# Optimization experiments

Measured on AMD Instinct MI355X. Metric: run time of the kernel, lower is better.

Reference implementation:

```python
import jax, jax.numpy as jnp
import numpy as np

B, S, E = 2048, 23, 768
RED, H, NUM_LABELS = 256, 8, 25
DH = RED // H
DELTA = 0.1
EPS_LN = 1e-5


def setup_inputs() -> dict:
    key = jax.random.key(0)
    ks = jax.random.split(key, 20)
    g = lambda k, shape, fan: jax.random.normal(k, shape, dtype=jnp.float32) * (1.0 / np.sqrt(fan))
    inp = {
        'cls_embeddings': jax.random.normal(ks[0], (B, S, E), dtype=jnp.float32),
        'existing_mask': jax.random.randint(ks[1], (B, S), 0, 2, dtype=jnp.int32),
        'missing_emb': g(ks[2], (S, E), E),
        'W1': g(ks[3], (E // 2, E), E), 'b1': jnp.zeros((E // 2,), jnp.float32),
        'W2': g(ks[4], (RED, E // 2), E // 2), 'b2': jnp.zeros((RED,), jnp.float32),
        'ln_g': jnp.ones((RED,), jnp.float32), 'ln_b': jnp.zeros((RED,), jnp.float32),
        'Wq': g(ks[5], (RED, RED), RED), 'bq': jnp.zeros((RED,), jnp.float32),
        'Wk': g(ks[6], (RED, RED), RED), 'bk': jnp.zeros((RED,), jnp.float32),
        'Wv': g(ks[7], (RED, RED), RED), 'bv': jnp.zeros((RED,), jnp.float32),
        'Wo': g(ks[8], (RED, RED), RED), 'bo': jnp.zeros((RED,), jnp.float32),
        'Wp': g(ks[9], (NUM_LABELS, RED), RED), 'bp': jnp.zeros((NUM_LABELS,), jnp.float32),
    }
    return inp


def _layer_norm(x, g, b):
    mu = jnp.mean(x, axis=-1, keepdims=True)
    var = jnp.mean(jnp.square(x - mu), axis=-1, keepdims=True)
    return (x - mu) * jax.lax.rsqrt(var + EPS_LN) * g + b


def _forward(cls_embeddings, existing_mask, missing_emb, W1, b1, W2, b2, ln_g, ln_b,
             Wq, bq, Wk, bk, Wv, bv, Wo, bo, Wp, bp):
    exist = existing_mask > 0                              # [B,S] bool
    # Gather: existing sections use BERT CLS, missing slots use learned embeddings
    sec = jnp.where(exist[..., None], cls_embeddings, missing_emb[None])  # [B,S,E]
    # SectionDimReducer (exact-erf GELU as in nn.GELU default)
    h = jax.nn.gelu(sec @ W1.T + b1, approximate=False)
    h = jax.nn.gelu(h @ W2.T + b2, approximate=False)
    red = _layer_norm(h, ln_g, ln_b)                       # [B,S,RED]
    # Tiny MHA: every slot queries the existing sections of its own EHR
    q = (red @ Wq.T + bq).reshape(B, S, H, DH)
    k = (red @ Wk.T + bk).reshape(B, S, H, DH)
    v = (red @ Wv.T + bv).reshape(B, S, H, DH)
    scores = jnp.einsum('bqhd,bkhd->bhqk', q, k) / np.sqrt(DH)
    scores = jnp.where(exist[:, None, None, :], scores, -1e9)
    attn = jax.nn.softmax(scores, axis=-1)                 # [B,H,S,S]
    ctx = jnp.einsum('bhqk,bkhd->bqhd', attn, v).reshape(B, S, RED)
    mha_out = ctx @ Wo.T + bo                              # [B,S,RED]
    # Scatter: only missing slots (of EHRs with >=1 existing section) are replaced
    any_exist = jnp.any(exist, axis=1)                     # [B]
    use_attn = (~exist) & any_exist[:, None]               # [B,S]
    updated = jnp.where(use_attn[..., None], mha_out, red)
    # margin-based orthogonality loss on section embeddings
    norm = updated / jnp.maximum(jnp.linalg.norm(updated, axis=-1, keepdims=True), 1e-8)
    gram = jnp.einsum('bid,bjd->bij', norm, norm)          # [B,S,S]
    off = 1.0 - jnp.eye(S, dtype=updated.dtype)
    loss_orth = jnp.sum(jax.nn.relu(jnp.abs(gram) - DELTA) * off) / (B * S * (S - 1))
    logits = updated.mean(axis=1) @ Wp.T + bp              # [B,NUM_LABELS]
    return loss_orth, logits


def reference(cls_embeddings, existing_mask, missing_emb, W1, b1, W2, b2, ln_g, ln_b,
              Wq, bq, Wk, bk, Wv, bv, Wo, bo, Wp, bp):
    return _forward(cls_embeddings, existing_mask, missing_emb, W1, b1, W2, b2, ln_g, ln_b,
                    Wq, bq, Wk, bk, Wv, bv, Wo, bo, Wp, bp)
```

## Files before the change

### kernel.cpp

```cpp
#include <hip/hip_runtime.h>

typedef unsigned short u16;
typedef unsigned int u32;
typedef __attribute__((ext_vector_type(8))) short short8;
typedef __attribute__((ext_vector_type(4))) float f32x4;

struct __align__(8) us4 { u16 x, y, z, w; };

__device__ __forceinline__ float bf1(u16 v){ return __uint_as_float(((u32)v) << 16); }
__device__ __forceinline__ float bflo(u32 u){ return __uint_as_float(u << 16); }
__device__ __forceinline__ float bfhi(u32 u){ return __uint_as_float(u & 0xFFFF0000u); }
__device__ __forceinline__ u16 fbf(float f){
    u32 u = __float_as_uint(f);
    return (u16)((u + 0x7FFFu + ((u >> 16) & 1u)) >> 16);
}
__device__ __forceinline__ float gelu_exact(float x){
    return 0.5f * x * (1.0f + erff(x * 0.70710678118654752f));
}
__device__ __forceinline__ void unp8(uint4 u, float* f){
    f[0]=bflo(u.x); f[1]=bfhi(u.x); f[2]=bflo(u.y); f[3]=bfhi(u.y);
    f[4]=bflo(u.z); f[5]=bfhi(u.z); f[6]=bflo(u.w); f[7]=bfhi(u.w);
}
__device__ __forceinline__ uint4 pack8(float4 a, float4 b){
    uint4 u;
    u.x = (u32)fbf(a.x) | ((u32)fbf(a.y) << 16);
    u.y = (u32)fbf(a.z) | ((u32)fbf(a.w) << 16);
    u.z = (u32)fbf(b.x) | ((u32)fbf(b.y) << 16);
    u.w = (u32)fbf(b.z) | ((u32)fbf(b.w) << 16);
    return u;
}


__global__ __launch_bounds__(256) void wconv(
    const float* __restrict__ W1, const float* __restrict__ W2,
    const float* __restrict__ Wq, const float* __restrict__ Wk,
    const float* __restrict__ Wv, const float* __restrict__ Wo,
    const float* __restrict__ Wp, u16* __restrict__ dst)
{
    const int i = blockIdx.x * 256 + threadIdx.x;
    const float* s; int o;
    if      (i < 294912) { s = W1; o = i; }
    else if (i < 393216) { s = W2; o = i - 294912; }
    else if (i < 458752) { s = Wq; o = i - 393216; }
    else if (i < 524288) { s = Wk; o = i - 458752; }
    else if (i < 589824) { s = Wv; o = i - 524288; }
    else if (i < 655360) { s = Wo; o = i - 589824; }
    else                 { s = Wp; o = i - 655360; }
    dst[i] = fbf(s[o]);
}

__global__ __launch_bounds__(256) void gemm1_kernel(
    const float* __restrict__ cls, const int* __restrict__ mask,
    const float* __restrict__ missing, const u16* __restrict__ W,
    const float* __restrict__ bias, u16* __restrict__ C)
{
    const int K = 768, M = 384;
    __shared__ u16 As[128 * 40];
    __shared__ u16 Bs[128 * 40];
    const int tid = threadIdx.x;
    const int w = tid >> 6, lane = tid & 63;
    const int nBase = blockIdx.y * 128, mBase = blockIdx.x * 128;
    const int wr = w >> 1, wc = w & 1;
    const int r0 = tid >> 2;
    const int co = (tid & 3) * 8;
    const int frow = lane & 15, quad = lane >> 4;

    const int rowA0 = nBase + r0, rowA1 = nBase + r0 + 64;
    const float* ap0 = (mask[rowA0] > 0) ? cls + (size_t)rowA0 * 768
                                         : missing + (size_t)(rowA0 % 23) * 768;
    const float* ap1 = (mask[rowA1] > 0) ? cls + (size_t)rowA1 * 768
                                         : missing + (size_t)(rowA1 % 23) * 768;
    const u16* bp0 = W + (size_t)(mBase + r0) * K;
    const u16* bp1 = W + (size_t)(mBase + r0 + 64) * K;

    f32x4 acc[4][4];
#pragma unroll
    for (int mt = 0; mt < 4; ++mt)
#pragma unroll
        for (int nt = 0; nt < 4; ++nt) acc[mt][nt] = f32x4{0.f, 0.f, 0.f, 0.f};

    float4 a0a = *(const float4*)(ap0 + co), a0b = *(const float4*)(ap0 + co + 4);
    float4 a1a = *(const float4*)(ap1 + co), a1b = *(const float4*)(ap1 + co + 4);
    uint4 pb0 = *(const uint4*)(bp0 + co), pb1 = *(const uint4*)(bp1 + co);

    for (int k0 = 0; k0 < K; k0 += 32) {
        __syncthreads();
        *(uint4*)(As + r0 * 40 + co) = pack8(a0a, a0b);
        *(uint4*)(As + (r0 + 64) * 40 + co) = pack8(a1a, a1b);
        *(uint4*)(Bs + r0 * 40 + co) = pb0;
        *(uint4*)(Bs + (r0 + 64) * 40 + co) = pb1;
        __syncthreads();
        if (k0 + 32 < K) {
            const int kn = k0 + 32 + co;
            a0a = *(const float4*)(ap0 + kn); a0b = *(const float4*)(ap0 + kn + 4);
            a1a = *(const float4*)(ap1 + kn); a1b = *(const float4*)(ap1 + kn + 4);
            pb0 = *(const uint4*)(bp0 + kn);  pb1 = *(const uint4*)(bp1 + kn);
        }
        short8 af[4], bfv[4];
#pragma unroll
        for (int mt = 0; mt < 4; ++mt)
            af[mt] = *(const short8*)(As + (wr * 64 + mt * 16 + frow) * 40 + quad * 8);
#pragma unroll
        for (int nt = 0; nt < 4; ++nt)
            bfv[nt] = *(const short8*)(Bs + (wc * 64 + nt * 16 + frow) * 40 + quad * 8);
#pragma unroll
        for (int mt = 0; mt < 4; ++mt)
#pragma unroll
            for (int nt = 0; nt < 4; ++nt)
                acc[mt][nt] = __builtin_amdgcn_mfma_f32_16x16x32_bf16(
                    af[mt], bfv[nt], acc[mt][nt], 0, 0, 0);
    }

#pragma unroll
    for (int nt = 0; nt < 4; ++nt) {
        const int col = mBase + wc * 64 + nt * 16 + frow;
        const float bv = bias[col];
#pragma unroll
        for (int mt = 0; mt < 4; ++mt)
#pragma unroll
            for (int reg = 0; reg < 4; ++reg) {
                const int row = nBase + wr * 64 + mt * 16 + quad * 4 + reg;
                C[(size_t)row * M + col] = fbf(gelu_exact(acc[mt][nt][reg] + bv));
            }
    }
}

__global__ __launch_bounds__(256) void gemm_bt(
    const u16* __restrict__ A, const u16* __restrict__ W,
    const float* __restrict__ bias, u16* __restrict__ C, int K, int M)
{
    __shared__ u16 As[128 * 40];
    __shared__ u16 Bs[128 * 40];
    const int tid = threadIdx.x;
    const int w = tid >> 6, lane = tid & 63;
    const int nBase = blockIdx.y * 128, mBase = blockIdx.x * 128;
    const int wr = w >> 1, wc = w & 1;
    const int r0 = tid >> 2;
    const int co = (tid & 3) * 8;
    const int frow = lane & 15, quad = lane >> 4;

    f32x4 acc[4][4];
#pragma unroll
    for (int mt = 0; mt < 4; ++mt)
#pragma unroll
        for (int nt = 0; nt < 4; ++nt) acc[mt][nt] = f32x4{0.f, 0.f, 0.f, 0.f};

    uint4 pa0 = *(const uint4*)(A + (size_t)(nBase + r0) * K + co);
    uint4 pa1 = *(const uint4*)(A + (size_t)(nBase + r0 + 64) * K + co);
    uint4 pb0 = *(const uint4*)(W + (size_t)(mBase + r0) * K + co);
    uint4 pb1 = *(const uint4*)(W + (size_t)(mBase + r0 + 64) * K + co);

    for (int k0 = 0; k0 < K; k0 += 32) {
        __syncthreads();
        *(uint4*)(As + r0 * 40 + co) = pa0;
        *(uint4*)(As + (r0 + 64) * 40 + co) = pa1;
        *(uint4*)(Bs + r0 * 40 + co) = pb0;
        *(uint4*)(Bs + (r0 + 64) * 40 + co) = pb1;
        __syncthreads();
        if (k0 + 32 < K) {
            const int kn = k0 + 32 + co;
            pa0 = *(const uint4*)(A + (size_t)(nBase + r0) * K + kn);
            pa1 = *(const uint4*)(A + (size_t)(nBase + r0 + 64) * K + kn);
            pb0 = *(const uint4*)(W + (size_t)(mBase + r0) * K + kn);
            pb1 = *(const uint4*)(W + (size_t)(mBase + r0 + 64) * K + kn);
        }
        short8 af[4], bfv[4];
#pragma unroll
        for (int mt = 0; mt < 4; ++mt)
            af[mt] = *(const short8*)(As + (wr * 64 + mt * 16 + frow) * 40 + quad * 8);
#pragma unroll
        for (int nt = 0; nt < 4; ++nt)
            bfv[nt] = *(const short8*)(Bs + (wc * 64 + nt * 16 + frow) * 40 + quad * 8);
#pragma unroll
        for (int mt = 0; mt < 4; ++mt)
#pragma unroll
            for (int nt = 0; nt < 4; ++nt)
                acc[mt][nt] = __builtin_amdgcn_mfma_f32_16x16x32_bf16(
                    af[mt], bfv[nt], acc[mt][nt], 0, 0, 0);
    }

#pragma unroll
    for (int nt = 0; nt < 4; ++nt) {
        const int col = mBase + wc * 64 + nt * 16 + frow;
        const float bv = bias[col];
#pragma unroll
        for (int mt = 0; mt < 4; ++mt)
#pragma unroll
            for (int reg = 0; reg < 4; ++reg) {
                const int row = nBase + wr * 64 + mt * 16 + quad * 4 + reg;
                C[(size_t)row * M + col] = fbf(gelu_exact(acc[mt][nt][reg] + bv));
            }
    }
}

__global__ __launch_bounds__(256) void ln_kernel(
    u16* __restrict__ X, const float* __restrict__ g, const float* __restrict__ b)
{
    const int w = threadIdx.x >> 6, lane = threadIdx.x & 63;
    const size_t row = (size_t)blockIdx.x * 4 + w;
    u16* xp = X + row * 256 + lane * 4;
    us4 uv = *(const us4*)xp;
    float x0 = bf1(uv.x), x1 = bf1(uv.y), x2 = bf1(uv.z), x3 = bf1(uv.w);
    float s = x0 + x1 + x2 + x3;
#pragma unroll
    for (int m = 32; m; m >>= 1) s += __shfl_xor(s, m);
    const float mu = s * (1.f / 256.f);
    const float d0 = x0 - mu, d1 = x1 - mu, d2 = x2 - mu, d3 = x3 - mu;
    float vs = d0 * d0 + d1 * d1 + d2 * d2 + d3 * d3;
#pragma unroll
    for (int m = 32; m; m >>= 1) vs += __shfl_xor(vs, m);
    const float rs = rsqrtf(vs * (1.f / 256.f) + 1e-5f);
    const float4 gv = *(const float4*)(g + lane * 4);
    const float4 bv = *(const float4*)(b + lane * 4);
    us4 o;
    o.x = fbf(d0 * rs * gv.x + bv.x);
    o.y = fbf(d1 * rs * gv.y + bv.y);
    o.z = fbf(d2 * rs * gv.z + bv.z);
    o.w = fbf(d3 * rs * gv.w + bv.w);
    *(us4*)xp = o;
}

#define QSTR 264
__global__ __launch_bounds__(256) void attn_tail_kernel(
    const u16* __restrict__ redb, const int* __restrict__ mask,
    const u16* __restrict__ Wqkvb,
    const float* __restrict__ bq, const float* __restrict__ bk,
    const float* __restrict__ bv, const u16* __restrict__ Wob,
    const float* __restrict__ bo, const u16* __restrict__ Wpb,
    const float* __restrict__ bp, float* __restrict__ out,
    float* __restrict__ lossAcc)
{
    __shared__ __align__(16) unsigned char SM[40960];
    u16* s_rq = (u16*)SM;
    u16* s_k  = (u16*)(SM + 12144);
    u16* s_vT = (u16*)(SM + 24288);
    int* sEx   = (int*)(SM + 40672);
    int* sMiss = (int*)(SM + 40764);
    float* sInv  = (float*)(SM + 24288);
    float* sPool = (float*)(SM + 24384);
    float* sRsc  = (float*)(SM + 25472);

    const int b = blockIdx.x, t = threadIdx.x;
    const int w = t >> 6, lane = t & 63;
    const int frow = lane & 15, quad = lane >> 4;
    const int r0c = frow;
    const int r1c = (16 + frow > 22) ? 22 : 16 + frow;

    {
        const int myEx = (t < 23) ? mask[b * 23 + t] : 0;
        if (t < 23) sEx[t] = myEx;
        if (t < 64) {
            const unsigned long long ball = __ballot((t < 23) && (myEx > 0));
            if (t < 23) sMiss[t] = (ball != 0ull && myEx <= 0) ? 1 : 0;
        }
    }
    for (int i = t; i < 1024; i += 256) ((uint4*)s_vT)[i] = make_uint4(0u, 0u, 0u, 0u);
    for (int i = t; i < 736; i += 256) {
        const int s = i >> 5, c8 = (i & 31) * 8;
        *(uint4*)(s_rq + s * QSTR + c8) =
            *(const uint4*)(redb + ((size_t)(b * 23 + s)) * 256 + c8);
    }
    __syncthreads();

    {
        f32x4 qacc[2][12];
#pragma unroll
        for (int mt = 0; mt < 2; ++mt)
#pragma unroll
            for (int nt = 0; nt < 12; ++nt) qacc[mt][nt] = f32x4{0.f, 0.f, 0.f, 0.f};
        for (int k0 = 0; k0 < 256; k0 += 32) {
            short8 a0 = *(const short8*)(s_rq + r0c * QSTR + k0 + quad * 8);
            short8 a1 = *(const short8*)(s_rq + r1c * QSTR + k0 + quad * 8);
#pragma unroll
            for (int nt = 0; nt < 12; ++nt) {
                const int n = (nt >> 2) * 256 + w * 64 + (nt & 3) * 16 + frow;
                short8 bfr = *(const short8*)(Wqkvb + (size_t)n * 256 + k0 + quad * 8);
                qacc[0][nt] = __builtin_amdgcn_mfma_f32_16x16x32_bf16(a0, bfr, qacc[0][nt], 0, 0, 0);
                qacc[1][nt] = __builtin_amdgcn_mfma_f32_16x16x32_bf16(a1, bfr, qacc[1][nt], 0, 0, 0);
            }
        }
        __syncthreads();
#pragma unroll
        for (int nt = 0; nt < 12; ++nt) {
            const int seg = nt >> 2;
            const int cm = w * 64 + (nt & 3) * 16 + frow;
            const float bb = (seg == 0) ? bq[cm] : (seg == 1) ? bk[cm] : bv[cm];
#pragma unroll
            for (int mt = 0; mt < 2; ++mt)
#pragma unroll
                for (int reg = 0; reg < 4; ++reg) {
                    const int s = mt * 16 + quad * 4 + reg;
                    if (s < 23) {
                        const u16 hv = fbf(qacc[mt][nt][reg] + bb);
                        if (seg == 0)      s_rq[s * QSTR + cm] = hv;
                        else if (seg == 1) s_k[s * QSTR + cm] = hv;
                        else               s_vT[cm * 32 + s] = hv;
                    }
                }
        }
    }

    {
        const float scl = 0.17677669529663687f;
        const float m0 = (sEx[frow] > 0) ? 0.f : -1e9f;
        const float m1 = (16 + frow < 23 && sEx[16 + frow] > 0) ? 0.f : -1e9f;
        const f32x4 z4 = f32x4{0.f, 0.f, 0.f, 0.f};
#pragma unroll
        for (int hh2 = 0; hh2 < 2; ++hh2) {
            const int hb = w * 64 + hh2 * 32;
            short8 aq0 = *(const short8*)(s_rq + r0c * QSTR + hb + quad * 8);
            short8 aq1 = *(const short8*)(s_rq + r1c * QSTR + hb + quad * 8);
            short8 bk0 = *(const short8*)(s_k + r0c * QSTR + hb + quad * 8);
            short8 bk1 = *(const short8*)(s_k + r1c * QSTR + hb + quad * 8);
            f32x4 s00 = __builtin_amdgcn_mfma_f32_16x16x32_bf16(aq0, bk0, z4, 0, 0, 0);
            f32x4 s01 = __builtin_amdgcn_mfma_f32_16x16x32_bf16(aq0, bk1, z4, 0, 0, 0);
            f32x4 s10 = __builtin_amdgcn_mfma_f32_16x16x32_bf16(aq1, bk0, z4, 0, 0, 0);
            f32x4 s11 = __builtin_amdgcn_mfma_f32_16x16x32_bf16(aq1, bk1, z4, 0, 0, 0);
#pragma unroll
            for (int mt = 0; mt < 2; ++mt) {
                f32x4& c0 = mt ? s10 : s00;
                f32x4& c1 = mt ? s11 : s01;
#pragma unroll
                for (int reg = 0; reg < 4; ++reg) {
                    float v0 = c0[reg] * scl + m0;
                    float v1 = c1[reg] * scl + m1;
                    float mx = fmaxf(v0, v1);
#pragma unroll
                    for (int m = 8; m; m >>= 1) mx = fmaxf(mx, __shfl_xor(mx, m));
                    float p0 = __expf(v0 - mx), p1 = __expf(v1 - mx);
                    float sm = p0 + p1;
#pragma unroll
                    for (int m = 8; m; m >>= 1) sm += __shfl_xor(sm, m);
                    const float inv = 1.f / sm;
                    c0[reg] = p0 * inv;
                    c1[reg] = p1 * inv;
                }
            }
#pragma unroll
            for (int reg = 0; reg < 4; ++reg) {
                const int q0r = quad * 4 + reg;
                s_k[q0r * QSTR + hb + frow]      = fbf(s00[reg]);
                s_k[q0r * QSTR + hb + 16 + frow] = fbf(s01[reg]);
                const int q1r = 16 + quad * 4 + reg;
                if (q1r < 23) {
                    s_k[q1r * QSTR + hb + frow]      = fbf(s10[reg]);
                    s_k[q1r * QSTR + hb + 16 + frow] = fbf(s11[reg]);
                }
            }
            short8 pa0 = *(const short8*)(s_k + r0c * QSTR + hb + quad * 8);
            short8 pa1 = *(const short8*)(s_k + r1c * QSTR + hb + quad * 8);
            short8 bv0 = *(const short8*)(s_vT + (hb + frow) * 32 + quad * 8);
            short8 bv1 = *(const short8*)(s_vT + (hb + 16 + frow) * 32 + quad * 8);
            f32x4 c00 = __builtin_amdgcn_mfma_f32_16x16x32_bf16(pa0, bv0, z4, 0, 0, 0);
            f32x4 c01 = __builtin_amdgcn_mfma_f32_16x16x32_bf16(pa0, bv1, z4, 0, 0, 0);
            f32x4 c10 = __builtin_amdgcn_mfma_f32_16x16x32_bf16(pa1, bv0, z4, 0, 0, 0);
            f32x4 c11 = __builtin_amdgcn_mfma_f32_16x16x32_bf16(pa1, bv1, z4, 0, 0, 0);
#pragma unroll
            for (int reg = 0; reg < 4; ++reg) {
                const int q0r = quad * 4 + reg;
                s_rq[q0r * QSTR + hb + frow]      = fbf(c00[reg]);
                s_rq[q0r * QSTR + hb + 16 + frow] = fbf(c01[reg]);
                const int q1r = 16 + quad * 4 + reg;
                if (q1r < 23) {
                    s_rq[q1r * QSTR + hb + frow]      = fbf(c10[reg]);
                    s_rq[q1r * QSTR + hb + 16 + frow] = fbf(c11[reg]);
                }
            }
        }
    }
    __syncthreads();

    {
        f32x4 wacc[2][4];
#pragma unroll
        for (int mt = 0; mt < 2; ++mt)
#pragma unroll
            for (int nt = 0; nt < 4; ++nt) wacc[mt][nt] = f32x4{0.f, 0.f, 0.f, 0.f};
        for (int k0 = 0; k0 < 256; k0 += 32) {
            short8 a0 = *(const short8*)(s_rq + r0c * QSTR + k0 + quad * 8);
            short8 a1 = *(const short8*)(s_rq + r1c * QSTR + k0 + quad * 8);
#pragma unroll
            for (int nt = 0; nt < 4; ++nt) {
                const int n = w * 64 + nt * 16 + frow;
                short8 bfr = *(const short8*)(Wob + (size_t)n * 256 + k0 + quad * 8);
                wacc[0][nt] = __builtin_amdgcn_mfma_f32_16x16x32_bf16(a0, bfr, wacc[0][nt], 0, 0, 0);
                wacc[1][nt] = __builtin_amdgcn_mfma_f32_16x16x32_bf16(a1, bfr, wacc[1][nt], 0, 0, 0);
            }
        }
        for (int i = t; i < 736; i += 256) {
            const int s = i >> 5;
            if (!sMiss[s]) {
                const int c8 = (i & 31) * 8;
                *(uint4*)(s_k + s * QSTR + c8) =
                    *(const uint4*)(redb + ((size_t)(b * 23 + s)) * 256 + c8);
            }
        }
#pragma unroll
        for (int nt = 0; nt < 4; ++nt) {
            const int col = w * 64 + nt * 16 + frow;
            const float bvv = bo[col];
#pragma unroll
            for (int mt = 0; mt < 2; ++mt)
#pragma unroll
                for (int reg = 0; reg < 4; ++reg) {
                    const int s = mt * 16 + quad * 4 + reg;
                    if (s < 23 && sMiss[s])
                        s_k[s * QSTR + col] = fbf(wacc[mt][nt][reg] + bvv);
                }
        }
    }
    __syncthreads();

    if (t < 23) {
        float ss = 0.f;
        for (int c8 = 0; c8 < 32; ++c8) {
            float rf[8]; unp8(*(const uint4*)(s_k + t * QSTR + c8 * 8), rf);
#pragma unroll
            for (int e = 0; e < 8; ++e) ss += rf[e] * rf[e];
        }
        sInv[t] = 1.f / fmaxf(sqrtf(ss), 1e-8f);
    }
    __syncthreads();

    {
        float contrib = 0.f;
        if (t < 253) {
            int i = 0, rem = t, cnt = 22;
            while (rem >= cnt) { rem -= cnt; --cnt; ++i; }
            const int j = i + 1 + rem;
            float dp = 0.f;
            for (int c8 = 0; c8 < 32; ++c8) {
                float fa[8], fb[8];
                unp8(*(const uint4*)(s_k + i * QSTR + c8 * 8), fa);
                unp8(*(const uint4*)(s_k + j * QSTR + c8 * 8), fb);
#pragma unroll
                for (int e = 0; e < 8; ++e) dp += fa[e] * fb[e];
            }
            const float g = dp * sInv[i] * sInv[j];
            const float c = fabsf(g) - 0.1f;
            contrib = (c > 0.f) ? 2.f * c : 0.f;
        }
#pragma unroll
        for (int m = 32; m; m >>= 1) contrib += __shfl_xor(contrib, m);
        if (lane == 0) sRsc[w] = contrib;

        float pv = 0.f;
#pragma unroll
        for (int s = 0; s < 23; ++s) pv += bf1(s_k[s * QSTR + t]);
        sPool[t] = pv * (1.f / 23.f);
    }
    __syncthreads();

    if (t == 0) atomicAdd(lossAcc, sRsc[0] + sRsc[1] + sRsc[2] + sRsc[3]);
    if (t < 25) {
        float a = bp[t];
        for (int c8 = 0; c8 < 32; ++c8) {
            float wf[8]; unp8(*(const uint4*)(Wpb + (size_t)t * 256 + c8 * 8), wf);
            const float4 p0 = *(const float4*)(sPool + c8 * 8);
            const float4 p1 = *(const float4*)(sPool + c8 * 8 + 4);
            a += wf[0] * p0.x + wf[1] * p0.y + wf[2] * p0.z + wf[3] * p0.w
               + wf[4] * p1.x + wf[5] * p1.y + wf[6] * p1.z + wf[7] * p1.w;
        }
        out[1 + b * 25 + t] = a;
    }
}

__global__ void loss_finalize(const float* __restrict__ lossAcc, float* __restrict__ out)
{
    out[0] = lossAcc[0] * (1.f / 1036288.f);
}

extern "C" void kernel_launch(void* const* d_in, const int* in_sizes, int n_in,
                              void* d_out, int out_size, void* d_ws, size_t ws_size,
                              hipStream_t stream)
{
    const float* cls     = (const float*)d_in[0];
    const int*   mask    = (const int*)d_in[1];
    const float* missing = (const float*)d_in[2];
    const float* W1 = (const float*)d_in[3];  const float* b1 = (const float*)d_in[4];
    const float* W2 = (const float*)d_in[5];  const float* b2 = (const float*)d_in[6];
    const float* lng = (const float*)d_in[7]; const float* lnb = (const float*)d_in[8];
    const float* Wq = (const float*)d_in[9];  const float* bq = (const float*)d_in[10];
    const float* Wk = (const float*)d_in[11]; const float* bk = (const float*)d_in[12];
    const float* Wv = (const float*)d_in[13]; const float* bv = (const float*)d_in[14];
    const float* Wo = (const float*)d_in[15]; const float* bo = (const float*)d_in[16];
    const float* Wp = (const float*)d_in[17]; const float* bp = (const float*)d_in[18];
    float* out = (float*)d_out;

    char* ws = (char*)d_ws;
    u16* h1b  = (u16*)ws;
    u16* redb = (u16*)(ws + 36175872);
    u16* Wb   = (u16*)(ws + 60293120);
    u16* W1b   = Wb;
    u16* W2b   = Wb + 294912;
    u16* Wqkvb = Wb + 393216;
    u16* Wob   = Wb + 589824;
    u16* Wpb   = Wb + 655360;
    float* lossAcc = (float*)(ws + 61616640);

    hipMemsetAsync(lossAcc, 0, sizeof(float), stream);

    wconv<<<2585, 256, 0, stream>>>(W1, W2, Wq, Wk, Wv, Wo, Wp, Wb);
    gemm1_kernel<<<dim3(3, 368), 256, 0, stream>>>(cls, mask, missing, W1b, b1, h1b);
    gemm_bt<<<dim3(2, 368), 256, 0, stream>>>(h1b, W2b, b2, redb, 384, 256);
    ln_kernel<<<11776, 256, 0, stream>>>(redb, lng, lnb);
    attn_tail_kernel<<<2048, 256, 0, stream>>>(redb, mask, Wqkvb, bq, bk, bv,
                                               Wob, bo, Wpb, bp, out, lossAcc);
    loss_finalize<<<1, 1, 0, stream>>>(lossAcc, out);
}
```

Before: 564.0 us.

## Fuse LayerNorm into attention tail and compute Gram matrix with MFMA

Removes the standalone LayerNorm kernel and applies LayerNorm inside the attention tail, once on the staged rows in shared memory and again on a reloaded copy of the rows before the final mix. The orthogonality Gram matrix and its diagonal norms now come from MFMA in one wavefront, replacing the per-thread scalar dot products, while the other waves compute pooling and logits in parallel. The QKV projection is split into three separate accumulator sets to cut register pressure, and the reload of the residual rows is issued before the Wo GEMM so its latency overlaps. In exchange, LayerNorm is computed twice per block and several extra barriers are added.

```diff
diff --git a/kernel.cpp b/kernel.cpp
--- a/kernel.cpp
+++ b/kernel.cpp
@@ -29,6 +29,9 @@
     u.w = (u32)fbf(b.z) | ((u32)fbf(b.w) << 16);
     return u;
 }
+
+#define MFMA16(a, b, c) __builtin_amdgcn_mfma_f32_16x16x32_bf16(a, b, c, 0, 0, 0)
+#define QSTR 264
 
 
 __global__ __launch_bounds__(256) void wconv(
@@ -107,8 +110,7 @@
         for (int mt = 0; mt < 4; ++mt)
 #pragma unroll
             for (int nt = 0; nt < 4; ++nt)
-                acc[mt][nt] = __builtin_amdgcn_mfma_f32_16x16x32_bf16(
-                    af[mt], bfv[nt], acc[mt][nt], 0, 0, 0);
+                acc[mt][nt] = MFMA16(af[mt], bfv[nt], acc[mt][nt]);
     }
 
 #pragma unroll
@@ -175,8 +177,7 @@
         for (int mt = 0; mt < 4; ++mt)
 #pragma unroll
             for (int nt = 0; nt < 4; ++nt)
-                acc[mt][nt] = __builtin_amdgcn_mfma_f32_16x16x32_bf16(
-                    af[mt], bfv[nt], acc[mt][nt], 0, 0, 0);
+                acc[mt][nt] = MFMA16(af[mt], bfv[nt], acc[mt][nt]);
     }
 
 #pragma unroll
@@ -193,40 +194,52 @@
     }
 }
 
-__global__ __launch_bounds__(256) void ln_kernel(
-    u16* __restrict__ X, const float* __restrict__ g, const float* __restrict__ b)
+__device__ __forceinline__ void ln_rows_inplace(
+    u16* base, int t, const float* __restrict__ lng, const float* __restrict__ lnb)
 {
-    const int w = threadIdx.x >> 6, lane = threadIdx.x & 63;
-    const size_t row = (size_t)blockIdx.x * 4 + w;
-    u16* xp = X + row * 256 + lane * 4;
-    us4 uv = *(const us4*)xp;
-    float x0 = bf1(uv.x), x1 = bf1(uv.y), x2 = bf1(uv.z), x3 = bf1(uv.w);
-    float s = x0 + x1 + x2 + x3;
-#pragma unroll
-    for (int m = 32; m; m >>= 1) s += __shfl_xor(s, m);
+    const int r = t >> 3, sub = t & 7;
+    if (r >= 23) return;
+    u16* rp = base + r * QSTR + sub * 32;
+    float x[32];
+    unp8(((const uint4*)rp)[0], x);
+    unp8(((const uint4*)rp)[1], x + 8);
+    unp8(((const uint4*)rp)[2], x + 16);
+    unp8(((const uint4*)rp)[3], x + 24);
+    float s = 0.f;
+#pragma unroll
+    for (int e = 0; e < 32; ++e) s += x[e];
+    s += __shfl_xor(s, 1); s += __shfl_xor(s, 2); s += __shfl_xor(s, 4);
     const float mu = s * (1.f / 256.f);
-    const float d0 = x0 - mu, d1 = x1 - mu, d2 = x2 - mu, d3 = x3 - mu;
-    float vs = d0 * d0 + d1 * d1 + d2 * d2 + d3 * d3;
-#pragma unroll
-    for (int m = 32; m; m >>= 1) vs += __shfl_xor(vs, m);
+    float vs = 0.f;
+#pragma unroll
+    for (int e = 0; e < 32; ++e) { const float d = x[e] - mu; vs += d * d; }
+    vs += __shfl_xor(vs, 1); vs += __shfl_xor(vs, 2); vs += __shfl_xor(vs, 4);
     const float rs = rsqrtf(vs * (1.f / 256.f) + 1e-5f);
-    const float4 gv = *(const float4*)(g + lane * 4);
-    const float4 bv = *(const float4*)(b + lane * 4);
-    us4 o;
-    o.x = fbf(d0 * rs * gv.x + bv.x);
-    o.y = fbf(d1 * rs * gv.y + bv.y);
-    o.z = fbf(d2 * rs * gv.z + bv.z);
-    o.w = fbf(d3 * rs * gv.w + bv.w);
-    *(us4*)xp = o;
-}
-
-#define QSTR 264
+#pragma unroll
+    for (int c8 = 0; c8 < 4; ++c8) {
+        const int cb = sub * 32 + c8 * 8;
+        const float4 g0 = *(const float4*)(lng + cb), g1 = *(const float4*)(lng + cb + 4);
+        const float4 b0 = *(const float4*)(lnb + cb), b1 = *(const float4*)(lnb + cb + 4);
+        float4 ya, yb;
+        ya.x = (x[c8*8+0]-mu)*rs*g0.x + b0.x;
+        ya.y = (x[c8*8+1]-mu)*rs*g0.y + b0.y;
+        ya.z = (x[c8*8+2]-mu)*rs*g0.z + b0.z;
+        ya.w = (x[c8*8+3]-mu)*rs*g0.w + b0.w;
+        yb.x = (x[c8*8+4]-mu)*rs*g1.x + b1.x;
+        yb.y = (x[c8*8+5]-mu)*rs*g1.y + b1.y;
+        yb.z = (x[c8*8+6]-mu)*rs*g1.z + b1.z;
+        yb.w = (x[c8*8+7]-mu)*rs*g1.w + b1.w;
+        ((uint4*)rp)[c8] = pack8(ya, yb);
+    }
+}
+
 __global__ __launch_bounds__(256) void attn_tail_kernel(
     const u16* __restrict__ redb, const int* __restrict__ mask,
     const u16* __restrict__ Wqkvb,
     const float* __restrict__ bq, const float* __restrict__ bk,
     const float* __restrict__ bv, const u16* __restrict__ Wob,
-    const float* __restrict__ bo, const u16* __restrict__ Wpb,
+    const float* __restrict__ bo, const float* __restrict__ lng,
+    const float* __restrict__ lnb, const u16* __restrict__ Wpb,
     const float* __restrict__ bp, float* __restrict__ out,
     float* __restrict__ lossAcc)
 {
@@ -236,15 +249,16 @@
     u16* s_vT = (u16*)(SM + 24288);
     int* sEx   = (int*)(SM + 40672);
     int* sMiss = (int*)(SM + 40764);
-    float* sInv  = (float*)(SM + 24288);
-    float* sPool = (float*)(SM + 24384);
-    float* sRsc  = (float*)(SM + 25472);
+    float* sDiag = (float*)(SM + 24288);
+    float* sInv  = (float*)(SM + 24384);
+    float* sPool = (float*)(SM + 24480);
 
     const int b = blockIdx.x, t = threadIdx.x;
     const int w = t >> 6, lane = t & 63;
     const int frow = lane & 15, quad = lane >> 4;
     const int r0c = frow;
     const int r1c = (16 + frow > 22) ? 22 : 16 + frow;
+    const f32x4 z4 = f32x4{0.f, 0.f, 0.f, 0.f};
 
     {
         const int myEx = (t < 23) ? mask[b * 23 + t] : 0;
@@ -262,40 +276,80 @@
     }
     __syncthreads();
 
+    ln_rows_inplace(s_rq, t, lng, lnb);
+    __syncthreads();
+
+#define QKV_KLOOP(SEGBASE, ACC)                                                   \
+    for (int k0 = 0; k0 < 256; k0 += 32) {                                        \
+        short8 a0 = *(const short8*)(s_rq + r0c * QSTR + k0 + quad * 8);          \
+        short8 a1 = *(const short8*)(s_rq + r1c * QSTR + k0 + quad * 8);          \
+        _Pragma("unroll")                                                         \
+        for (int nt = 0; nt < 4; ++nt) {                                          \
+            const int n = (SEGBASE) + w * 64 + nt * 16 + frow;                    \
+            short8 bfr = *(const short8*)(Wqkvb + (size_t)n * 256 + k0 + quad * 8); \
+            ACC[0][nt] = MFMA16(a0, bfr, ACC[0][nt]);                             \
+            ACC[1][nt] = MFMA16(a1, bfr, ACC[1][nt]);                             \
+        }                                                                         \
+    }
+
     {
-        f32x4 qacc[2][12];
+        f32x4 ka[2][4];
 #pragma unroll
         for (int mt = 0; mt < 2; ++mt)
 #pragma unroll
-            for (int nt = 0; nt < 12; ++nt) qacc[mt][nt] = f32x4{0.f, 0.f, 0.f, 0.f};
-        for (int k0 = 0; k0 < 256; k0 += 32) {
-            short8 a0 = *(const short8*)(s_rq + r0c * QSTR + k0 + quad * 8);
-            short8 a1 = *(const short8*)(s_rq + r1c * QSTR + k0 + quad * 8);
-#pragma unroll
-            for (int nt = 0; nt < 12; ++nt) {
-                const int n = (nt >> 2) * 256 + w * 64 + (nt & 3) * 16 + frow;
-                short8 bfr = *(const short8*)(Wqkvb + (size_t)n * 256 + k0 + quad * 8);
-                qacc[0][nt] = __builtin_amdgcn_mfma_f32_16x16x32_bf16(a0, bfr, qacc[0][nt], 0, 0, 0);
-                qacc[1][nt] = __builtin_amdgcn_mfma_f32_16x16x32_bf16(a1, bfr, qacc[1][nt], 0, 0, 0);
-            }
-        }
-        __syncthreads();
-#pragma unroll
-        for (int nt = 0; nt < 12; ++nt) {
-            const int seg = nt >> 2;
-            const int cm = w * 64 + (nt & 3) * 16 + frow;
-            const float bb = (seg == 0) ? bq[cm] : (seg == 1) ? bk[cm] : bv[cm];
+            for (int nt = 0; nt < 4; ++nt) ka[mt][nt] = z4;
+        QKV_KLOOP(256, ka)
+#pragma unroll
+        for (int nt = 0; nt < 4; ++nt) {
+            const int cm = w * 64 + nt * 16 + frow;
+            const float bb = bk[cm];
 #pragma unroll
             for (int mt = 0; mt < 2; ++mt)
 #pragma unroll
                 for (int reg = 0; reg < 4; ++reg) {
                     const int s = mt * 16 + quad * 4 + reg;
-                    if (s < 23) {
-                        const u16 hv = fbf(qacc[mt][nt][reg] + bb);
-                        if (seg == 0)      s_rq[s * QSTR + cm] = hv;
-                        else if (seg == 1) s_k[s * QSTR + cm] = hv;
-                        else               s_vT[cm * 32 + s] = hv;
-                    }
+                    if (s < 23) s_k[s * QSTR + cm] = fbf(ka[mt][nt][reg] + bb);
+                }
+        }
+    }
+    {
+        f32x4 va[2][4];
+#pragma unroll
+        for (int mt = 0; mt < 2; ++mt)
+#pragma unroll
+            for (int nt = 0; nt < 4; ++nt) va[mt][nt] = z4;
+        QKV_KLOOP(512, va)
+#pragma unroll
+        for (int nt = 0; nt < 4; ++nt) {
+            const int cm = w * 64 + nt * 16 + frow;
+            const float bb = bv[cm];
+#pragma unroll
+            for (int mt = 0; mt < 2; ++mt)
+#pragma unroll
+                for (int reg = 0; reg < 4; ++reg) {
+                    const int s = mt * 16 + quad * 4 + reg;
+                    if (s < 23) s_vT[cm * 32 + s] = fbf(va[mt][nt][reg] + bb);
+                }
+        }
+    }
+    {
+        f32x4 qa[2][4];
+#pragma unroll
+        for (int mt = 0; mt < 2; ++mt)
+#pragma unroll
+            for (int nt = 0; nt < 4; ++nt) qa[mt][nt] = z4;
+        QKV_KLOOP(0, qa)
+        __syncthreads();
+#pragma unroll
+        for (int nt = 0; nt < 4; ++nt) {
+            const int cm = w * 64 + nt * 16 + frow;
+            const float bb = bq[cm];
+#pragma unroll
+            for (int mt = 0; mt < 2; ++mt)
+#pragma unroll
+                for (int reg = 0; reg < 4; ++reg) {
+                    const int s = mt * 16 + quad * 4 + reg;
+                    if (s < 23) s_rq[s * QSTR + cm] = fbf(qa[mt][nt][reg] + bb);
                 }
         }
     }
@@ -304,7 +358,6 @@
         const float scl = 0.17677669529663687f;
         const float m0 = (sEx[frow] > 0) ? 0.f : -1e9f;
         const float m1 = (16 + frow < 23 && sEx[16 + frow] > 0) ? 0.f : -1e9f;
-        const f32x4 z4 = f32x4{0.f, 0.f, 0.f, 0.f};
 #pragma unroll
         for (int hh2 = 0; hh2 < 2; ++hh2) {
             const int hb = w * 64 + hh2 * 32;
@@ -312,10 +365,10 @@
             short8 aq1 = *(const short8*)(s_rq + r1c * QSTR + hb + quad * 8);
             short8 bk0 = *(const short8*)(s_k + r0c * QSTR + hb + quad * 8);
             short8 bk1 = *(const short8*)(s_k + r1c * QSTR + hb + quad * 8);
-            f32x4 s00 = __builtin_amdgcn_mfma_f32_16x16x32_bf16(aq0, bk0, z4, 0, 0, 0);
-            f32x4 s01 = __builtin_amdgcn_mfma_f32_16x16x32_bf16(aq0, bk1, z4, 0, 0, 0);
-            f32x4 s10 = __builtin_amdgcn_mfma_f32_16x16x32_bf16(aq1, bk0, z4, 0, 0, 0);
-            f32x4 s11 = __builtin_amdgcn_mfma_f32_16x16x32_bf16(aq1, bk1, z4, 0, 0, 0);
+            f32x4 s00 = MFMA16(aq0, bk0, z4);
+            f32x4 s01 = MFMA16(aq0, bk1, z4);
+            f32x4 s10 = MFMA16(aq1, bk0, z4);
+            f32x4 s11 = MFMA16(aq1, bk1, z4);
 #pragma unroll
             for (int mt = 0; mt < 2; ++mt) {
                 f32x4& c0 = mt ? s10 : s00;
@@ -351,10 +404,10 @@
             short8 pa1 = *(const short8*)(s_k + r1c * QSTR + hb + quad * 8);
             short8 bv0 = *(const short8*)(s_vT + (hb + frow) * 32 + quad * 8);
             short8 bv1 = *(const short8*)(s_vT + (hb + 16 + frow) * 32 + quad * 8);
-            f32x4 c00 = __builtin_amdgcn_mfma_f32_16x16x32_bf16(pa0, bv0, z4, 0, 0, 0);
-            f32x4 c01 = __builtin_amdgcn_mfma_f32_16x16x32_bf16(pa0, bv1, z4, 0, 0, 0);
-            f32x4 c10 = __builtin_amdgcn_mfma_f32_16x16x32_bf16(pa1, bv0, z4, 0, 0, 0);
-            f32x4 c11 = __builtin_amdgcn_mfma_f32_16x16x32_bf16(pa1, bv1, z4, 0, 0, 0);
+            f32x4 c00 = MFMA16(pa0, bv0, z4);
+            f32x4 c01 = MFMA16(pa0, bv1, z4);
+            f32x4 c10 = MFMA16(pa1, bv0, z4);
+            f32x4 c11 = MFMA16(pa1, bv1, z4);
 #pragma unroll
             for (int reg = 0; reg < 4; ++reg) {
                 const int q0r = quad * 4 + reg;
@@ -371,11 +424,19 @@
     __syncthreads();
 
     {
+        const u16* src = redb + (size_t)(b * 23) * 256;
+        const int s0 = t >> 5, c0o = (t & 31) * 8;
+        uint4 rg0 = *(const uint4*)(src + s0 * 256 + c0o);
+        uint4 rg1 = *(const uint4*)(src + (s0 + 8) * 256 + c0o);
+        uint4 rg2;
+        const bool has2 = (t + 512) < 736;
+        if (has2) rg2 = *(const uint4*)(src + (s0 + 16) * 256 + c0o);
+
         f32x4 wacc[2][4];
 #pragma unroll
         for (int mt = 0; mt < 2; ++mt)
 #pragma unroll
-            for (int nt = 0; nt < 4; ++nt) wacc[mt][nt] = f32x4{0.f, 0.f, 0.f, 0.f};
+            for (int nt = 0; nt < 4; ++nt) wacc[mt][nt] = z4;
         for (int k0 = 0; k0 < 256; k0 += 32) {
             short8 a0 = *(const short8*)(s_rq + r0c * QSTR + k0 + quad * 8);
             short8 a1 = *(const short8*)(s_rq + r1c * QSTR + k0 + quad * 8);
@@ -383,18 +444,16 @@
             for (int nt = 0; nt < 4; ++nt) {
                 const int n = w * 64 + nt * 16 + frow;
                 short8 bfr = *(const short8*)(Wob + (size_t)n * 256 + k0 + quad * 8);
-                wacc[0][nt] = __builtin_amdgcn_mfma_f32_16x16x32_bf16(a0, bfr, wacc[0][nt], 0, 0, 0);
-                wacc[1][nt] = __builtin_amdgcn_mfma_f32_16x16x32_bf16(a1, bfr, wacc[1][nt], 0, 0, 0);
-            }
-        }
-        for (int i = t; i < 736; i += 256) {
-            const int s = i >> 5;
-            if (!sMiss[s]) {
-                const int c8 = (i & 31) * 8;
-                *(uint4*)(s_k + s * QSTR + c8) =
-                    *(const uint4*)(redb + ((size_t)(b * 23 + s)) * 256 + c8);
-            }
-        }
+                wacc[0][nt] = MFMA16(a0, bfr, wacc[0][nt]);
+                wacc[1][nt] = MFMA16(a1, bfr, wacc[1][nt]);
+            }
+        }
+        *(uint4*)(s_k + s0 * QSTR + c0o) = rg0;
+        *(uint4*)(s_k + (s0 + 8) * QSTR + c0o) = rg1;
+        if (has2) *(uint4*)(s_k + (s0 + 16) * QSTR + c0o) = rg2;
+        __syncthreads();
+        ln_rows_inplace(s_k, t, lng, lnb);
+        __syncthreads();
 #pragma unroll
         for (int nt = 0; nt < 4; ++nt) {
             const int col = w * 64 + nt * 16 + frow;
@@ -411,57 +470,88 @@
     }
     __syncthreads();
 
-    if (t < 23) {
-        float ss = 0.f;
-        for (int c8 = 0; c8 < 32; ++c8) {
-            float rf[8]; unp8(*(const uint4*)(s_k + t * QSTR + c8 * 8), rf);
-#pragma unroll
-            for (int e = 0; e < 8; ++e) ss += rf[e] * rf[e];
-        }
-        sInv[t] = 1.f / fmaxf(sqrtf(ss), 1e-8f);
+    f32x4 g00 = z4, g01 = z4, g10 = z4, g11 = z4;
+    if (w == 0) {
+        for (int k0 = 0; k0 < 256; k0 += 32) {
+            short8 a0 = *(const short8*)(s_k + r0c * QSTR + k0 + quad * 8);
+            short8 a1 = *(const short8*)(s_k + r1c * QSTR + k0 + quad * 8);
+            g00 = MFMA16(a0, a0, g00);
+            g01 = MFMA16(a0, a1, g01);
+            g10 = MFMA16(a1, a0, g10);
+            g11 = MFMA16(a1, a1, g11);
+        }
+#pragma unroll
+        for (int reg = 0; reg < 4; ++reg) {
+            if (frow == quad * 4 + reg) {
+                sDiag[frow] = g00[reg];
+                if (16 + frow < 23) sDiag[16 + frow] = g11[reg];
+            }
+        }
+    } else {
+        for (int c = t - 64; c < 256; c += 192) {
+            float pv = 0.f;
+#pragma unroll
+            for (int s = 0; s < 23; ++s) pv += bf1(s_k[s * QSTR + c]);
+            sPool[c] = pv * (1.f / 23.f);
+        }
     }
     __syncthreads();
-
-    {
+    if (t < 23) sInv[t] = 1.f / fmaxf(sqrtf(sDiag[t]), 1e-8f);
+    __syncthreads();
+
+    if (w == 0) {
         float contrib = 0.f;
-        if (t < 253) {
-            int i = 0, rem = t, cnt = 22;
-            while (rem >= cnt) { rem -= cnt; --cnt; ++i; }
-            const int j = i + 1 + rem;
-            float dp = 0.f;
-            for (int c8 = 0; c8 < 32; ++c8) {
-                float fa[8], fb[8];
-                unp8(*(const uint4*)(s_k + i * QSTR + c8 * 8), fa);
-                unp8(*(const uint4*)(s_k + j * QSTR + c8 * 8), fb);
-#pragma unroll
-                for (int e = 0; e < 8; ++e) dp += fa[e] * fb[e];
-            }
-            const float g = dp * sInv[i] * sInv[j];
-            const float c = fabsf(g) - 0.1f;
-            contrib = (c > 0.f) ? 2.f * c : 0.f;
+        const float ic0 = sInv[frow];
+        const float ic1 = (16 + frow < 23) ? sInv[16 + frow] : 0.f;
+        const bool c1ok = (16 + frow < 23);
+#pragma unroll
+        for (int reg = 0; reg < 4; ++reg) {
+            const int rA = quad * 4 + reg;
+            const float irA = sInv[rA];
+            if (rA != frow) {
+                const float cc = fabsf(g00[reg] * irA * ic0) - 0.1f;
+                if (cc > 0.f) contrib += cc;
+            }
+            if (c1ok) {
+                const float cc = fabsf(g01[reg] * irA * ic1) - 0.1f;
+                if (cc > 0.f) contrib += cc;
+            }
+            const int rB = 16 + quad * 4 + reg;
+            if (rB < 23) {
+                const float irB = sInv[rB];
+                {
+                    const float cc = fabsf(g10[reg] * irB * ic0) - 0.1f;
+                    if (cc > 0.f) contrib += cc;
+                }
+                if (c1ok && rB != 16 + frow) {
+                    const float cc = fabsf(g11[reg] * irB * ic1) - 0.1f;
+                    if (cc > 0.f) contrib += cc;
+                }
+            }
         }
 #pragma unroll
         for (int m = 32; m; m >>= 1) contrib += __shfl_xor(contrib, m);
-        if (lane == 0) sRsc[w] = contrib;
-
-        float pv = 0.f;
-#pragma unroll
-        for (int s = 0; s < 23; ++s) pv += bf1(s_k[s * QSTR + t]);
-        sPool[t] = pv * (1.f / 23.f);
-    }
-    __syncthreads();
-
-    if (t == 0) atomicAdd(lossAcc, sRsc[0] + sRsc[1] + sRsc[2] + sRsc[3]);
-    if (t < 25) {
-        float a = bp[t];
-        for (int c8 = 0; c8 < 32; ++c8) {
-            float wf[8]; unp8(*(const uint4*)(Wpb + (size_t)t * 256 + c8 * 8), wf);
-            const float4 p0 = *(const float4*)(sPool + c8 * 8);
-            const float4 p1 = *(const float4*)(sPool + c8 * 8 + 4);
-            a += wf[0] * p0.x + wf[1] * p0.y + wf[2] * p0.z + wf[3] * p0.w
-               + wf[4] * p1.x + wf[5] * p1.y + wf[6] * p1.z + wf[7] * p1.w;
-        }
-        out[1 + b * 25 + t] = a;
+        if (lane == 0) atomicAdd(lossAcc, contrib);
+    } else {
+        const int li = t - 64;
+#pragma unroll 1
+        for (int pass = 0; pass < 2; ++pass) {
+            int L, chunk;
+            if (pass == 0) { L = li >> 3; chunk = li & 7; }
+            else { if (li >= 8) break; L = 24; chunk = li; }
+            float a = 0.f;
+#pragma unroll
+            for (int q4 = 0; q4 < 4; ++q4) {
+                const int c8 = chunk * 4 + q4;
+                float wf[8]; unp8(*(const uint4*)(Wpb + (size_t)L * 256 + c8 * 8), wf);
+                const float4 p0 = *(const float4*)(sPool + c8 * 8);
+                const float4 p1 = *(const float4*)(sPool + c8 * 8 + 4);
+                a += wf[0] * p0.x + wf[1] * p0.y + wf[2] * p0.z + wf[3] * p0.w
+                   + wf[4] * p1.x + wf[5] * p1.y + wf[6] * p1.z + wf[7] * p1.w;
+            }
+            a += __shfl_xor(a, 1); a += __shfl_xor(a, 2); a += __shfl_xor(a, 4);
+            if (chunk == 0) out[1 + b * 25 + L] = a + bp[L];
+        }
     }
 }
 
@@ -503,8 +593,8 @@
     wconv<<<2585, 256, 0, stream>>>(W1, W2, Wq, Wk, Wv, Wo, Wp, Wb);
     gemm1_kernel<<<dim3(3, 368), 256, 0, stream>>>(cls, mask, missing, W1b, b1, h1b);
     gemm_bt<<<dim3(2, 368), 256, 0, stream>>>(h1b, W2b, b2, redb, 384, 256);
-    ln_kernel<<<11776, 256, 0, stream>>>(redb, lng, lnb);
     attn_tail_kernel<<<2048, 256, 0, stream>>>(redb, mask, Wqkvb, bq, bk, bv,
-                                               Wob, bo, Wpb, bp, out, lossAcc);
+                                               Wob, bo, lng, lnb, Wpb, bp,
+                                               out, lossAcc);
     loss_finalize<<<1, 1, 0, stream>>>(lossAcc, out);
 }
```

New measurement: 550.5 us. 2.4% less time.
